# Optimization experiments

Hardware: AMD Instinct MI355X
Metric: run time of the kernel (lower is better)

## Reference

```python
import jax, jax.numpy as jnp
import numpy as np

N = 100000
E = 1600000
G = 256
D_IN = 128
NEURON = 64
ATT_F = 8
K = 3
ALPHA = 0.1


def setup_inputs() -> dict:
    key = jax.random.key(0)
    ks = jax.random.split(key, 12)
    x = jax.random.normal(ks[0], (N, D_IN), dtype=jnp.float32)
    closeness_feature = jax.random.normal(ks[1], (N, ATT_F), dtype=jnp.float32)
    edge_index = jax.random.randint(ks[2], (2, E), 0, N, dtype=jnp.int32)
    batch = jnp.sort(jax.random.randint(ks[3], (N,), 0, G, dtype=jnp.int32))
    s = 0.05
    return {
        "x": x,
        "closeness_feature": closeness_feature,
        "edge_index": edge_index,
        "batch": batch,
        "num_graphs": G,
        "nn1_w": jax.random.normal(ks[4], (D_IN, NEURON), dtype=jnp.float32) * s,
        "nn1_b": jnp.zeros((NEURON,), dtype=jnp.float32),
        "close_w": jax.random.normal(ks[5], (ATT_F, 1), dtype=jnp.float32) * s,
        "close_b": jnp.zeros((1,), dtype=jnp.float32),
        "att1_w": jax.random.normal(ks[6], (NEURON, 16), dtype=jnp.float32) * s,
        "att1_b": jnp.zeros((16,), dtype=jnp.float32),
        "att2_w": jax.random.normal(ks[7], (16, 1), dtype=jnp.float32) * s,
        "att2_b": jnp.zeros((1,), dtype=jnp.float32),
    }


def _appnp(x, edge_index, n):
    # gcn_norm with self-loops: A_hat = D^{-1/2}(A+I)D^{-1/2}
    loop = jnp.arange(n, dtype=edge_index.dtype)
    src = jnp.concatenate([edge_index[0], loop])
    dst = jnp.concatenate([edge_index[1], loop])
    deg = jax.ops.segment_sum(jnp.ones_like(dst, dtype=x.dtype), dst, num_segments=n)
    dinv = jax.lax.rsqrt(deg)  # deg >= 1 due to self loops
    norm = (dinv[src] * dinv[dst])[:, None]  # [E+N, 1]
    h = x
    for _ in range(K):
        agg = jax.ops.segment_sum(norm * h[src], dst, num_segments=n)
        h = (1.0 - ALPHA) * agg + ALPHA * x
    return h


def reference(x, closeness_feature, edge_index, batch, num_graphs,
              nn1_w, nn1_b, close_w, close_b, att1_w, att1_b, att2_w, att2_b):
    n = x.shape[0]
    h = _appnp(x, edge_index, n)                      # [N, D_IN]
    h = jax.nn.relu(h @ nn1_w + nn1_b)                # [N, 64]

    # per-graph softmax over closeness scores (segment softmax)
    logits = (closeness_feature @ close_w + close_b)[:, 0]          # [N]
    m = jax.ops.segment_max(logits, batch, num_segments=num_graphs)  # [G]
    w = jnp.exp(logits - m[batch])
    z = jax.ops.segment_sum(w, batch, num_segments=num_graphs)       # [G]
    p = w / z[batch]                                                 # softmax per graph

    cnt = jax.ops.segment_sum(jnp.ones((n,), dtype=h.dtype), batch,
                              num_segments=num_graphs)               # nodes per graph
    p = p * cnt[batch]                                               # scaled by curr_size

    # self_max: per-graph max over weighted node features
    pooled = jax.ops.segment_max(p[:, None] * h, batch, num_segments=num_graphs)  # [G, 64]

    a = jax.nn.relu(pooled @ att1_w + att1_b)         # [G, 16]
    return a @ att2_w + att2_b                        # [G, 1]
```

## Files before the change

### kernel.cpp

```cpp
#include <hip/hip_runtime.h>
#include <cstdint>
#include <cstddef>


#define DIN 128
#define NEU 64
#define BK2 512
#define BKSHIFT2 9
#define BKCAP 16384
#define ESCAP 12288
#define MAXNB 256

typedef __attribute__((ext_vector_type(8))) short short8v;
typedef __attribute__((ext_vector_type(4))) float f32x4;

__device__ inline float bf2f(unsigned short h) {
    return __uint_as_float(((unsigned)h) << 16);
}
__device__ inline unsigned short f2bf(float f) {
    unsigned u = __float_as_uint(f);
    unsigned r = u + 0x7FFFu + ((u >> 16) & 1u);
    return (unsigned short)(r >> 16);
}


__global__ __launch_bounds__(256) void binA_kernel(
        const int* __restrict__ src, const int* __restrict__ dst,
        int* __restrict__ bcur, int* __restrict__ pk, int E, int NB) {
    __shared__ int hist[MAXNB];
    __shared__ int cur[MAXNB];
    int nchunk = gridDim.x;
    int chunk = (E + nchunk - 1) / nchunk;
    int lo = blockIdx.x * chunk;
    int hi = min(E, lo + chunk);
    int t = threadIdx.x;
    for (int b = t; b < NB; b += 256) hist[b] = 0;
    __syncthreads();
    for (int i = lo + t; i < hi; i += 256)
        atomicAdd(&hist[dst[i] >> BKSHIFT2], 1);
    __syncthreads();
    for (int b = t; b < NB; b += 256)
        cur[b] = atomicAdd(&bcur[b], hist[b]);
    __syncthreads();
    for (int i = lo + t; i < hi; i += 256) {
        int d = dst[i];
        int b = d >> BKSHIFT2;
        int pos = atomicAdd(&cur[b], 1);
        pk[(size_t)b * BKCAP + pos] = (src[i] << BKSHIFT2) | (d & (BK2 - 1));
    }
}


__global__ void bscan_kernel(const int* __restrict__ bcur, int* __restrict__ bbase, int NB) {
    __shared__ int sh[256];
    int t = threadIdx.x;
    sh[t] = (t < NB) ? bcur[t] : 0;
    __syncthreads();
    for (int d = 1; d < 256; d <<= 1) {
        int v = (t >= d) ? sh[t - d] : 0;
        __syncthreads();
        sh[t] += v;
        __syncthreads();
    }
    if (t < NB) bbase[t + 1] = sh[t];
    if (t == 0) bbase[0] = 0;
}


__global__ __launch_bounds__(256) void binB_kernel(
        const int* __restrict__ bcur, const int* __restrict__ bbase,
        const int* __restrict__ pk, int* __restrict__ es,
        int* __restrict__ rowptr, float* __restrict__ dinv, int N, int NB) {
    __shared__ int cur[BK2];
    __shared__ int sh[256];
    __shared__ int esl[ESCAP];
    int b = blockIdx.x;
    int t = threadIdx.x;
    int node0 = b << BKSHIFT2;
    int count = bcur[b];
    int base = bbase[b];
    const int* pb = pk + (size_t)b * BKCAP;

    for (int v = t; v < BK2; v += 256) cur[v] = 0;
    __syncthreads();
    for (int i = t; i < count; i += 256)
        atomicAdd(&cur[pb[i] & (BK2 - 1)], 1);
    __syncthreads();
    int c0 = cur[2 * t], c1 = cur[2 * t + 1];
    int s = c0 + c1;
    sh[t] = s;
    __syncthreads();
    for (int d = 1; d < 256; d <<= 1) {
        int v = (t >= d) ? sh[t - d] : 0;
        __syncthreads();
        sh[t] += v;
        __syncthreads();
    }
    int excl = sh[t] - s;
    int n0 = node0 + 2 * t;
    if (n0 < N) {
        rowptr[n0 + 1] = base + excl + c0;
        dinv[n0] = rsqrtf((float)c0 + 1.0f);
    }
    if (n0 + 1 < N) {
        rowptr[n0 + 2] = base + excl + c0 + c1;
        dinv[n0 + 1] = rsqrtf((float)c1 + 1.0f);
    }
    if (b == 0 && t == 0) rowptr[0] = 0;
    __syncthreads();
    cur[2 * t] = excl;
    cur[2 * t + 1] = excl + c0;
    __syncthreads();
    for (int i = t; i < count; i += 256) {
        int v = pb[i];
        int pos = atomicAdd(&cur[v & (BK2 - 1)], 1);
        if (pos < ESCAP) esl[pos] = v >> BKSHIFT2;
    }
    __syncthreads();
    for (int i = t; i < count; i += 256) es[base + i] = esl[i];
}


__global__ __launch_bounds__(256) void fc1_kernel(
        const float* __restrict__ x, const float* __restrict__ W,
        ushort* __restrict__ yb, int N) {
    __shared__ ushort sW[DIN * NEU];
    int tid = threadIdx.x;
    for (int k = tid; k < DIN * NEU / 2; k += 256) {
        float2 v = ((const float2*)W)[k];
        ushort2 o;
        o.x = f2bf(v.x);
        o.y = f2bf(v.y);
        ((ushort2*)sW)[k] = o;
    }
    __syncthreads();
    int lane = tid & 63;
    int wv = tid >> 6;
    int l15 = lane & 15;
    int lg = lane >> 4;
    short8v bfrag[4][4];
#pragma unroll
    for (int kt = 0; kt < 4; kt++)
#pragma unroll
        for (int ct = 0; ct < 4; ct++) {
            short8v f;
#pragma unroll
            for (int e = 0; e < 8; e++)
                f[e] = (short)sW[(kt * 32 + lg * 8 + e) * NEU + ct * 16 + l15];
            bfrag[kt][ct] = f;
        }
    long long row0 = (long long)blockIdx.x * 64 + wv * 16;
    if (row0 >= N) return;
    bool rowok = (row0 + l15) < N;
    const float* xr = x + (size_t)(row0 + l15) * DIN;
    f32x4 acc[4];
#pragma unroll
    for (int ct = 0; ct < 4; ct++) acc[ct] = (f32x4){0.f, 0.f, 0.f, 0.f};
#pragma unroll
    for (int kt = 0; kt < 4; kt++) {
        short8v af = (short8v){0, 0, 0, 0, 0, 0, 0, 0};
        if (rowok) {
            float4 v0 = *((const float4*)(xr + kt * 32 + lg * 8));
            float4 v1 = *((const float4*)(xr + kt * 32 + lg * 8 + 4));
            af[0] = (short)f2bf(v0.x); af[1] = (short)f2bf(v0.y);
            af[2] = (short)f2bf(v0.z); af[3] = (short)f2bf(v0.w);
            af[4] = (short)f2bf(v1.x); af[5] = (short)f2bf(v1.y);
            af[6] = (short)f2bf(v1.z); af[7] = (short)f2bf(v1.w);
        }
#pragma unroll
        for (int ct = 0; ct < 4; ct++)
            acc[ct] = __builtin_amdgcn_mfma_f32_16x16x32_bf16(af, bfrag[kt][ct], acc[ct], 0, 0, 0);
    }
#pragma unroll
    for (int ct = 0; ct < 4; ct++)
#pragma unroll
        for (int r = 0; r < 4; r++) {
            long long rr = row0 + lg * 4 + r;
            if (rr < N) yb[(size_t)rr * NEU + ct * 16 + l15] = f2bf(acc[ct][r]);
        }
}


__global__ void scale_kernel(const ushort* __restrict__ yb, const float* __restrict__ dinv,
                             ushort* __restrict__ g0, ushort* __restrict__ g1,
                             ushort* __restrict__ g2, int N) {
    int i = blockIdx.x * blockDim.x + threadIdx.x;
    int stride = gridDim.x * blockDim.x;
    int total = N * 16;
    for (; i < total; i += stride) {
        int node = i >> 4;
        float dd = dinv[node];
        ushort4 v = ((const ushort4*)yb)[i];
        ushort4 o;
        o.x = f2bf(dd * bf2f(v.x));
        o.y = f2bf(dd * bf2f(v.y));
        o.z = f2bf(dd * bf2f(v.z));
        o.w = f2bf(dd * bf2f(v.w));
        ((ushort4*)g0)[i] = o;
    }
    if (blockIdx.x == 0 && threadIdx.x < 48) {
        int buf = threadIdx.x >> 4, e = threadIdx.x & 15;
        ushort* gp = (buf == 0) ? g0 : (buf == 1) ? g1 : g2;
        ((ushort4*)(gp + (size_t)N * NEU))[e] = make_ushort4(0, 0, 0, 0);
    }
}


template <int MODE>
__global__ __launch_bounds__(256) void pull_kernel(
        const int* __restrict__ rowptr, const int* __restrict__ es,
        const float* __restrict__ dinv, const ushort* __restrict__ gin,
        const ushort* __restrict__ yb, const float* __restrict__ b1,
        ushort* __restrict__ gout, float* __restrict__ h2out, int N) {
    int wid = threadIdx.x >> 6;
    int lane = threadIdx.x & 63;
    int quarter = lane >> 4;
    int l16 = lane & 15;
    int node = blockIdx.x * 4 + wid;
    if (node >= N) return;
    int beg = rowptr[node], end = rowptr[node + 1];
    float dd = dinv[node];
    float4 a0 = make_float4(0.f, 0.f, 0.f, 0.f);
    float4 a1 = make_float4(0.f, 0.f, 0.f, 0.f);
    float4 a2 = make_float4(0.f, 0.f, 0.f, 0.f);
    float4 a3 = make_float4(0.f, 0.f, 0.f, 0.f);
    int deg = end - beg;
    for (int base = 0; base < deg; base += 64) {
        int myi = base + lane;
        int msrc = (myi < deg) ? es[beg + myi] : N;
        int cnt = min(64, deg - base);
        int quads4 = (cnt + 15) >> 4;
        for (int j = 0; j < quads4; j++) {
            int i0 = 16 * j + quarter;
            int s0 = __shfl(msrc, i0);
            int s1 = __shfl(msrc, i0 + 4);
            int s2 = __shfl(msrc, i0 + 8);
            int s3 = __shfl(msrc, i0 + 12);
            ushort4 w0 = *((const ushort4*)(gin + (size_t)s0 * NEU) + l16);
            ushort4 w1 = *((const ushort4*)(gin + (size_t)s1 * NEU) + l16);
            ushort4 w2 = *((const ushort4*)(gin + (size_t)s2 * NEU) + l16);
            ushort4 w3 = *((const ushort4*)(gin + (size_t)s3 * NEU) + l16);
            a0.x += bf2f(w0.x); a0.y += bf2f(w0.y); a0.z += bf2f(w0.z); a0.w += bf2f(w0.w);
            a1.x += bf2f(w1.x); a1.y += bf2f(w1.y); a1.z += bf2f(w1.z); a1.w += bf2f(w1.w);
            a2.x += bf2f(w2.x); a2.y += bf2f(w2.y); a2.z += bf2f(w2.z); a2.w += bf2f(w2.w);
            a3.x += bf2f(w3.x); a3.y += bf2f(w3.y); a3.z += bf2f(w3.z); a3.w += bf2f(w3.w);
        }
    }
    float4 acc;
    acc.x = (a0.x + a1.x) + (a2.x + a3.x);
    acc.y = (a0.y + a1.y) + (a2.y + a3.y);
    acc.z = (a0.z + a1.z) + (a2.z + a3.z);
    acc.w = (a0.w + a1.w) + (a2.w + a3.w);
    acc.x += __shfl_xor(acc.x, 16);
    acc.y += __shfl_xor(acc.y, 16);
    acc.z += __shfl_xor(acc.z, 16);
    acc.w += __shfl_xor(acc.w, 16);
    acc.x += __shfl_xor(acc.x, 32);
    acc.y += __shfl_xor(acc.y, 32);
    acc.z += __shfl_xor(acc.z, 32);
    acc.w += __shfl_xor(acc.w, 32);
    if (quarter == 0) {
        ushort4 gv = *((const ushort4*)(gin + (size_t)node * NEU) + l16);
        ushort4 yv = *((const ushort4*)(yb + (size_t)node * NEU) + l16);
        float c9 = 0.9f * dd;
        float hx = c9 * (acc.x + bf2f(gv.x)) + 0.1f * bf2f(yv.x);
        float hy = c9 * (acc.y + bf2f(gv.y)) + 0.1f * bf2f(yv.y);
        float hz = c9 * (acc.z + bf2f(gv.z)) + 0.1f * bf2f(yv.z);
        float hw = c9 * (acc.w + bf2f(gv.w)) + 0.1f * bf2f(yv.w);
        if (MODE == 1) {
            float4 bb = *((const float4*)b1 + l16);
            float4 o;
            o.x = fmaxf(hx + bb.x, 0.f);
            o.y = fmaxf(hy + bb.y, 0.f);
            o.z = fmaxf(hz + bb.z, 0.f);
            o.w = fmaxf(hw + bb.w, 0.f);
            *((float4*)(h2out + (size_t)node * NEU) + l16) = o;
        } else {
            ushort4 o;
            o.x = f2bf(dd * hx); o.y = f2bf(dd * hy);
            o.z = f2bf(dd * hz); o.w = f2bf(dd * hw);
            *((ushort4*)(gout + (size_t)node * NEU) + l16) = o;
        }
    }
}


__global__ void logits_kernel(const float* __restrict__ cf, const float* __restrict__ cw,
                              const float* __restrict__ cb, float* __restrict__ logits, int N) {
    int i = blockIdx.x * blockDim.x + threadIdx.x;
    if (i >= N) return;
    const float4* c = (const float4*)(cf + (size_t)i * 8);
    float4 a = c[0], b = c[1];
    float s = a.x * cw[0] + a.y * cw[1] + a.z * cw[2] + a.w * cw[3]
            + b.x * cw[4] + b.y * cw[5] + b.z * cw[6] + b.w * cw[7] + cb[0];
    logits[i] = s;
}


__global__ void boundary_kernel(const int* __restrict__ batch, int* __restrict__ offs,
                                int N, int G) {
    int g = blockIdx.x * blockDim.x + threadIdx.x;
    if (g > G) return;
    int lo = 0, hi = N;
    while (lo < hi) {
        int mid = (lo + hi) >> 1;
        if (batch[mid] < g) lo = mid + 1; else hi = mid;
    }
    offs[g] = lo;
}


__global__ __launch_bounds__(256) void softmax_kernel(
        const float* __restrict__ logits, const int* __restrict__ offs,
        float* __restrict__ p, int G) {
    int g = blockIdx.x;
    int s0 = offs[g], e0 = offs[g + 1];
    int tid = threadIdx.x;
    __shared__ float red[256];
    float m = -INFINITY;
    for (int i = s0 + tid; i < e0; i += 256) m = fmaxf(m, logits[i]);
    red[tid] = m; __syncthreads();
    for (int w = 128; w > 0; w >>= 1) {
        if (tid < w) red[tid] = fmaxf(red[tid], red[tid + w]);
        __syncthreads();
    }
    m = red[0]; __syncthreads();
    float z = 0.f;
    for (int i = s0 + tid; i < e0; i += 256) z += expf(logits[i] - m);
    red[tid] = z; __syncthreads();
    for (int w = 128; w > 0; w >>= 1) {
        if (tid < w) red[tid] += red[tid + w];
        __syncthreads();
    }
    z = red[0];
    float scale = (float)(e0 - s0) / z;
    for (int i = s0 + tid; i < e0; i += 256) p[i] = expf(logits[i] - m) * scale;
}


__global__ __launch_bounds__(256) void pool_kernel(
        const float* __restrict__ h2, const float* __restrict__ p,
        const int* __restrict__ offs, float* __restrict__ pooled, int G) {
    int g = blockIdx.x;
    int s0 = offs[g], e0 = offs[g + 1];
    int tid = threadIdx.x;
    int j = tid & 63, r = tid >> 6;
    float mx = -INFINITY;
    for (int i = s0 + r; i < e0; i += 4)
        mx = fmaxf(mx, p[i] * h2[(size_t)i * NEU + j]);
    __shared__ float red[256];
    red[tid] = mx;
    __syncthreads();
    if (r == 0) {
        float m0 = fmaxf(fmaxf(red[j], red[64 + j]), fmaxf(red[128 + j], red[192 + j]));
        pooled[(size_t)g * NEU + j] = m0;
    }
}


__global__ void final_kernel(const float* __restrict__ pooled, const float* __restrict__ w1,
                             const float* __restrict__ b1, const float* __restrict__ w2,
                             const float* __restrict__ b2, float* __restrict__ out, int G) {
    int g = blockIdx.x;
    int tid = threadIdx.x;
    __shared__ float sp[64];
    __shared__ float sa[16];
    sp[tid] = pooled[(size_t)g * 64 + tid];
    __syncthreads();
    if (tid < 16) {
        float acc = b1[tid];
#pragma unroll
        for (int k = 0; k < 64; k++) acc = fmaf(sp[k], w1[k * 16 + tid], acc);
        sa[tid] = fmaxf(acc, 0.f);
    }
    __syncthreads();
    if (tid == 0) {
        float o = b2[0];
#pragma unroll
        for (int k = 0; k < 16; k++) o = fmaf(sa[k], w2[k], o);
        out[g] = o;
    }
}


extern "C" void kernel_launch(void* const* d_in, const int* in_sizes, int n_in,
                              void* d_out, int out_size, void* d_ws, size_t ws_size,
                              hipStream_t stream) {
    const float* x       = (const float*)d_in[0];
    const float* cf      = (const float*)d_in[1];
    const int*   ei      = (const int*)d_in[2];
    const int*   batch   = (const int*)d_in[3];
    const float* nn1_w   = (const float*)d_in[5];
    const float* nn1_b   = (const float*)d_in[6];
    const float* close_w = (const float*)d_in[7];
    const float* close_b = (const float*)d_in[8];
    const float* att1_w  = (const float*)d_in[9];
    const float* att1_b  = (const float*)d_in[10];
    const float* att2_w  = (const float*)d_in[11];
    const float* att2_b  = (const float*)d_in[12];
    float* out = (float*)d_out;

    int N = in_sizes[0] / DIN;
    int E = in_sizes[2] / 2;
    int G = out_size;

    const int* src = ei;
    const int* dst = ei + E;

    char* w = (char*)d_ws;
    size_t off = 0;
    auto alloc = [&](size_t bytes) -> void* {
        void* ptr = w + off;
        off += (bytes + 511) & ~(size_t)511;
        return ptr;
    };
    int NB = (N + BK2 - 1) >> BKSHIFT2;

    ushort* yb     = (ushort*)alloc((size_t)N * NEU * 2);
    ushort* g0     = (ushort*)alloc(((size_t)N + 1) * NEU * 2);
    ushort* g1     = (ushort*)alloc(((size_t)N + 1) * NEU * 2);
    ushort* g2     = (ushort*)alloc(((size_t)N + 1) * NEU * 2);
    float* h2      = (float*)alloc((size_t)N * NEU * 4);
    float* dinv    = (float*)alloc((size_t)N * 4);
    int*   rowptr  = (int*)alloc(((size_t)N + 1) * 4);
    int*   es      = (int*)alloc((size_t)E * 4);
    int*   bcur    = (int*)alloc((size_t)NB * 4);
    int*   bbase   = (int*)alloc(((size_t)NB + 1) * 4);
    int*   pk      = (int*)alloc((size_t)NB * BKCAP * 4);
    float* logits  = (float*)alloc((size_t)N * 4);
    float* p       = (float*)alloc((size_t)N * 4);
    int*   offs    = (int*)alloc(((size_t)G + 1) * 4);
    float* pooled  = (float*)alloc((size_t)G * NEU * 4);
    (void)ws_size; (void)n_in;

    hipMemsetAsync(bcur, 0, (size_t)NB * 4, stream);

    binA_kernel<<<256, 256, 0, stream>>>(src, dst, bcur, pk, E, NB);
    bscan_kernel<<<1, 256, 0, stream>>>(bcur, bbase, NB);
    binB_kernel<<<NB, 256, 0, stream>>>(bcur, bbase, pk, es, rowptr, dinv, N, NB);

    fc1_kernel<<<(N + 63) / 64, 256, 0, stream>>>(x, nn1_w, yb, N);
    scale_kernel<<<2048, 256, 0, stream>>>(yb, dinv, g0, g1, g2, N);

    pull_kernel<0><<<(N + 3) / 4, 256, 0, stream>>>(rowptr, es, dinv, g0, yb, nn1_b, g1, nullptr, N);
    pull_kernel<0><<<(N + 3) / 4, 256, 0, stream>>>(rowptr, es, dinv, g1, yb, nn1_b, g2, nullptr, N);
    pull_kernel<1><<<(N + 3) / 4, 256, 0, stream>>>(rowptr, es, dinv, g2, yb, nn1_b, nullptr, h2, N);

    logits_kernel<<<(N + 255) / 256, 256, 0, stream>>>(cf, close_w, close_b, logits, N);
    boundary_kernel<<<2, 256, 0, stream>>>(batch, offs, N, G);
    softmax_kernel<<<G, 256, 0, stream>>>(logits, offs, p, G);
    pool_kernel<<<G, 256, 0, stream>>>(h2, p, offs, pooled, G);
    final_kernel<<<G, 64, 0, stream>>>(pooled, att1_w, att1_b, att2_w, att2_b, out, G);
}
```

Before: 239.5 us.

## Fuse scale into fc1, merge head kernels, simplify pull gather unroll

Writes the dinv-scaled g0 directly from the fc1 epilogue, which removes the separate scale kernel and its reread of yb. Five head kernels (logits, boundary, softmax, pool, final) become one per-graph kernel that uses an online max/sum softmax and recomputes logits inline, cutting launches and intermediate buffers. The pull gather loop is narrowed from four to two independent loads per iteration and uses 32-bit indexing. This lowers memory-level parallelism in the gather, and the fast __expf adds some numerical risk.

```diff
diff --git a/kernel.cpp b/kernel.cpp
--- a/kernel.cpp
+++ b/kernel.cpp
@@ -123,9 +123,16 @@
 
 __global__ __launch_bounds__(256) void fc1_kernel(
         const float* __restrict__ x, const float* __restrict__ W,
-        ushort* __restrict__ yb, int N) {
+        const float* __restrict__ dinv, ushort* __restrict__ yb,
+        ushort* __restrict__ g0, ushort* __restrict__ g1,
+        ushort* __restrict__ g2, int N) {
+    int tid = threadIdx.x;
+    if (blockIdx.x == 0 && tid < 48) {
+        int buf = tid >> 4, e = tid & 15;
+        ushort* gp = (buf == 0) ? g0 : (buf == 1) ? g1 : g2;
+        ((ushort4*)(gp + (size_t)N * NEU))[e] = make_ushort4(0, 0, 0, 0);
+    }
     __shared__ ushort sW[DIN * NEU];
-    int tid = threadIdx.x;
     for (int k = tid; k < DIN * NEU / 2; k += 256) {
         float2 v = ((const float2*)W)[k];
         ushort2 o;
@@ -172,36 +179,17 @@
             acc[ct] = __builtin_amdgcn_mfma_f32_16x16x32_bf16(af, bfrag[kt][ct], acc[ct], 0, 0, 0);
     }
 #pragma unroll
-    for (int ct = 0; ct < 4; ct++)
-#pragma unroll
-        for (int r = 0; r < 4; r++) {
-            long long rr = row0 + lg * 4 + r;
-            if (rr < N) yb[(size_t)rr * NEU + ct * 16 + l15] = f2bf(acc[ct][r]);
-        }
-}
-
-
-__global__ void scale_kernel(const ushort* __restrict__ yb, const float* __restrict__ dinv,
-                             ushort* __restrict__ g0, ushort* __restrict__ g1,
-                             ushort* __restrict__ g2, int N) {
-    int i = blockIdx.x * blockDim.x + threadIdx.x;
-    int stride = gridDim.x * blockDim.x;
-    int total = N * 16;
-    for (; i < total; i += stride) {
-        int node = i >> 4;
-        float dd = dinv[node];
-        ushort4 v = ((const ushort4*)yb)[i];
-        ushort4 o;
-        o.x = f2bf(dd * bf2f(v.x));
-        o.y = f2bf(dd * bf2f(v.y));
-        o.z = f2bf(dd * bf2f(v.z));
-        o.w = f2bf(dd * bf2f(v.w));
-        ((ushort4*)g0)[i] = o;
-    }
-    if (blockIdx.x == 0 && threadIdx.x < 48) {
-        int buf = threadIdx.x >> 4, e = threadIdx.x & 15;
-        ushort* gp = (buf == 0) ? g0 : (buf == 1) ? g1 : g2;
-        ((ushort4*)(gp + (size_t)N * NEU))[e] = make_ushort4(0, 0, 0, 0);
+    for (int r = 0; r < 4; r++) {
+        long long rr = row0 + lg * 4 + r;
+        if (rr < N) {
+            float dv = dinv[rr];
+#pragma unroll
+            for (int ct = 0; ct < 4; ct++) {
+                float v = acc[ct][r];
+                yb[(size_t)rr * NEU + ct * 16 + l15] = f2bf(v);
+                g0[(size_t)rr * NEU + ct * 16 + l15] = f2bf(dv * v);
+            }
+        }
     }
 }
 
@@ -220,37 +208,35 @@
     if (node >= N) return;
     int beg = rowptr[node], end = rowptr[node + 1];
     float dd = dinv[node];
+    const ushort4* gin4 = (const ushort4*)gin;
     float4 a0 = make_float4(0.f, 0.f, 0.f, 0.f);
     float4 a1 = make_float4(0.f, 0.f, 0.f, 0.f);
-    float4 a2 = make_float4(0.f, 0.f, 0.f, 0.f);
-    float4 a3 = make_float4(0.f, 0.f, 0.f, 0.f);
     int deg = end - beg;
     for (int base = 0; base < deg; base += 64) {
         int myi = base + lane;
         int msrc = (myi < deg) ? es[beg + myi] : N;
         int cnt = min(64, deg - base);
-        int quads4 = (cnt + 15) >> 4;
-        for (int j = 0; j < quads4; j++) {
-            int i0 = 16 * j + quarter;
-            int s0 = __shfl(msrc, i0);
-            int s1 = __shfl(msrc, i0 + 4);
-            int s2 = __shfl(msrc, i0 + 8);
-            int s3 = __shfl(msrc, i0 + 12);
-            ushort4 w0 = *((const ushort4*)(gin + (size_t)s0 * NEU) + l16);
-            ushort4 w1 = *((const ushort4*)(gin + (size_t)s1 * NEU) + l16);
-            ushort4 w2 = *((const ushort4*)(gin + (size_t)s2 * NEU) + l16);
-            ushort4 w3 = *((const ushort4*)(gin + (size_t)s3 * NEU) + l16);
+        int quads = (cnt + 3) >> 2;
+        int j = 0;
+        for (; j + 1 < quads; j += 2) {
+            int s0 = __shfl(msrc, 4 * j + quarter);
+            int s1 = __shfl(msrc, 4 * j + 4 + quarter);
+            ushort4 w0 = gin4[(uint)(s0 << 4) + l16];
+            ushort4 w1 = gin4[(uint)(s1 << 4) + l16];
             a0.x += bf2f(w0.x); a0.y += bf2f(w0.y); a0.z += bf2f(w0.z); a0.w += bf2f(w0.w);
             a1.x += bf2f(w1.x); a1.y += bf2f(w1.y); a1.z += bf2f(w1.z); a1.w += bf2f(w1.w);
-            a2.x += bf2f(w2.x); a2.y += bf2f(w2.y); a2.z += bf2f(w2.z); a2.w += bf2f(w2.w);
-            a3.x += bf2f(w3.x); a3.y += bf2f(w3.y); a3.z += bf2f(w3.z); a3.w += bf2f(w3.w);
+        }
+        if (j < quads) {
+            int s0 = __shfl(msrc, 4 * j + quarter);
+            ushort4 w0 = gin4[(uint)(s0 << 4) + l16];
+            a0.x += bf2f(w0.x); a0.y += bf2f(w0.y); a0.z += bf2f(w0.z); a0.w += bf2f(w0.w);
         }
     }
     float4 acc;
-    acc.x = (a0.x + a1.x) + (a2.x + a3.x);
-    acc.y = (a0.y + a1.y) + (a2.y + a3.y);
-    acc.z = (a0.z + a1.z) + (a2.z + a3.z);
-    acc.w = (a0.w + a1.w) + (a2.w + a3.w);
+    acc.x = a0.x + a1.x;
+    acc.y = a0.y + a1.y;
+    acc.z = a0.z + a1.z;
+    acc.w = a0.w + a1.w;
     acc.x += __shfl_xor(acc.x, 16);
     acc.y += __shfl_xor(acc.y, 16);
     acc.z += __shfl_xor(acc.z, 16);
@@ -285,99 +271,86 @@
 }
 
 
-__global__ void logits_kernel(const float* __restrict__ cf, const float* __restrict__ cw,
-                              const float* __restrict__ cb, float* __restrict__ logits, int N) {
-    int i = blockIdx.x * blockDim.x + threadIdx.x;
-    if (i >= N) return;
-    const float4* c = (const float4*)(cf + (size_t)i * 8);
-    float4 a = c[0], b = c[1];
-    float s = a.x * cw[0] + a.y * cw[1] + a.z * cw[2] + a.w * cw[3]
-            + b.x * cw[4] + b.y * cw[5] + b.z * cw[6] + b.w * cw[7] + cb[0];
-    logits[i] = s;
-}
-
-
-__global__ void boundary_kernel(const int* __restrict__ batch, int* __restrict__ offs,
-                                int N, int G) {
-    int g = blockIdx.x * blockDim.x + threadIdx.x;
-    if (g > G) return;
-    int lo = 0, hi = N;
-    while (lo < hi) {
-        int mid = (lo + hi) >> 1;
-        if (batch[mid] < g) lo = mid + 1; else hi = mid;
-    }
-    offs[g] = lo;
-}
-
-
-__global__ __launch_bounds__(256) void softmax_kernel(
-        const float* __restrict__ logits, const int* __restrict__ offs,
-        float* __restrict__ p, int G) {
+__global__ __launch_bounds__(256) void head_kernel(
+        const int* __restrict__ batch, const float* __restrict__ cf,
+        const float* __restrict__ cw, const float* __restrict__ cb,
+        const float* __restrict__ h2, const float* __restrict__ aw1,
+        const float* __restrict__ ab1, const float* __restrict__ aw2,
+        const float* __restrict__ ab2, float* __restrict__ out, int N) {
     int g = blockIdx.x;
-    int s0 = offs[g], e0 = offs[g + 1];
     int tid = threadIdx.x;
-    __shared__ float red[256];
-    float m = -INFINITY;
-    for (int i = s0 + tid; i < e0; i += 256) m = fmaxf(m, logits[i]);
-    red[tid] = m; __syncthreads();
+    __shared__ int sbound[2];
+    __shared__ float redm[256];
+    __shared__ float redz[256];
+    __shared__ float pooled[64];
+    __shared__ float sa[16];
+    if (tid < 2) {
+        int target = g + tid;
+        int lo = 0, hi = N;
+        while (lo < hi) {
+            int mid = (lo + hi) >> 1;
+            if (batch[mid] < target) lo = mid + 1; else hi = mid;
+        }
+        sbound[tid] = lo;
+    }
+    __syncthreads();
+    int s0 = sbound[0], e0 = sbound[1];
+    float w0 = cw[0], w1 = cw[1], w2 = cw[2], w3 = cw[3];
+    float w4 = cw[4], w5 = cw[5], w6 = cw[6], w7 = cw[7];
+    float cb0 = cb[0];
+    float m = -INFINITY, z = 0.f;
+    for (int i = s0 + tid; i < e0; i += 256) {
+        const float4* c = (const float4*)(cf + (size_t)i * 8);
+        float4 A = c[0], B = c[1];
+        float l = A.x * w0 + A.y * w1 + A.z * w2 + A.w * w3
+                + B.x * w4 + B.y * w5 + B.z * w6 + B.w * w7 + cb0;
+        float mn = fmaxf(m, l);
+        z = z * __expf(m - mn) + __expf(l - mn);
+        m = mn;
+    }
+    redm[tid] = m; redz[tid] = z;
+    __syncthreads();
     for (int w = 128; w > 0; w >>= 1) {
-        if (tid < w) red[tid] = fmaxf(red[tid], red[tid + w]);
+        if (tid < w) {
+            float ma = redm[tid], mb = redm[tid + w];
+            float za = redz[tid], zb = redz[tid + w];
+            float mn = fmaxf(ma, mb);
+            redz[tid] = (mn == -INFINITY) ? 0.f
+                       : za * __expf(ma - mn) + zb * __expf(mb - mn);
+            redm[tid] = mn;
+        }
         __syncthreads();
     }
-    m = red[0]; __syncthreads();
-    float z = 0.f;
-    for (int i = s0 + tid; i < e0; i += 256) z += expf(logits[i] - m);
-    red[tid] = z; __syncthreads();
-    for (int w = 128; w > 0; w >>= 1) {
-        if (tid < w) red[tid] += red[tid + w];
-        __syncthreads();
-    }
-    z = red[0];
-    float scale = (float)(e0 - s0) / z;
-    for (int i = s0 + tid; i < e0; i += 256) p[i] = expf(logits[i] - m) * scale;
-}
-
-
-__global__ __launch_bounds__(256) void pool_kernel(
-        const float* __restrict__ h2, const float* __restrict__ p,
-        const int* __restrict__ offs, float* __restrict__ pooled, int G) {
-    int g = blockIdx.x;
-    int s0 = offs[g], e0 = offs[g + 1];
-    int tid = threadIdx.x;
+    float M = redm[0];
+    float scale = (float)(e0 - s0) / redz[0];
+    __syncthreads();
     int j = tid & 63, r = tid >> 6;
     float mx = -INFINITY;
-    for (int i = s0 + r; i < e0; i += 4)
-        mx = fmaxf(mx, p[i] * h2[(size_t)i * NEU + j]);
-    __shared__ float red[256];
-    red[tid] = mx;
-    __syncthreads();
-    if (r == 0) {
-        float m0 = fmaxf(fmaxf(red[j], red[64 + j]), fmaxf(red[128 + j], red[192 + j]));
-        pooled[(size_t)g * NEU + j] = m0;
-    }
-}
-
-
-__global__ void final_kernel(const float* __restrict__ pooled, const float* __restrict__ w1,
-                             const float* __restrict__ b1, const float* __restrict__ w2,
-                             const float* __restrict__ b2, float* __restrict__ out, int G) {
-    int g = blockIdx.x;
-    int tid = threadIdx.x;
-    __shared__ float sp[64];
-    __shared__ float sa[16];
-    sp[tid] = pooled[(size_t)g * 64 + tid];
+    for (int i = s0 + r; i < e0; i += 4) {
+        const float4* c = (const float4*)(cf + (size_t)i * 8);
+        float4 A = c[0], B = c[1];
+        float l = A.x * w0 + A.y * w1 + A.z * w2 + A.w * w3
+                + B.x * w4 + B.y * w5 + B.z * w6 + B.w * w7 + cb0;
+        float p = __expf(l - M) * scale;
+        mx = fmaxf(mx, p * h2[(size_t)i * NEU + j]);
+    }
+    redm[tid] = mx;
+    __syncthreads();
+    if (r == 0)
+        pooled[j] = fmaxf(fmaxf(redm[j], redm[64 + j]),
+                          fmaxf(redm[128 + j], redm[192 + j]));
     __syncthreads();
     if (tid < 16) {
-        float acc = b1[tid];
-#pragma unroll
-        for (int k = 0; k < 64; k++) acc = fmaf(sp[k], w1[k * 16 + tid], acc);
+        float acc = ab1[tid];
+#pragma unroll
+        for (int k = 0; k < 64; k++) acc = fmaf(pooled[k], aw1[k * 16 + tid], acc);
         sa[tid] = fmaxf(acc, 0.f);
     }
     __syncthreads();
     if (tid == 0) {
-        float o = b2[0];
-#pragma unroll
-        for (int k = 0; k < 16; k++) o = fmaf(sa[k], w2[k], o);
+        float o = ab2[0];
+#pragma unroll
+        for (int k = 0; k < 16; k++) o = fmaf(sa[k], aw2[k], o);
         out[g] = o;
     }
 }
@@ -427,10 +400,6 @@
     int*   bcur    = (int*)alloc((size_t)NB * 4);
     int*   bbase   = (int*)alloc(((size_t)NB + 1) * 4);
     int*   pk      = (int*)alloc((size_t)NB * BKCAP * 4);
-    float* logits  = (float*)alloc((size_t)N * 4);
-    float* p       = (float*)alloc((size_t)N * 4);
-    int*   offs    = (int*)alloc(((size_t)G + 1) * 4);
-    float* pooled  = (float*)alloc((size_t)G * NEU * 4);
     (void)ws_size; (void)n_in;
 
     hipMemsetAsync(bcur, 0, (size_t)NB * 4, stream);
@@ -439,16 +408,12 @@
     bscan_kernel<<<1, 256, 0, stream>>>(bcur, bbase, NB);
     binB_kernel<<<NB, 256, 0, stream>>>(bcur, bbase, pk, es, rowptr, dinv, N, NB);
 
-    fc1_kernel<<<(N + 63) / 64, 256, 0, stream>>>(x, nn1_w, yb, N);
-    scale_kernel<<<2048, 256, 0, stream>>>(yb, dinv, g0, g1, g2, N);
+    fc1_kernel<<<(N + 63) / 64, 256, 0, stream>>>(x, nn1_w, dinv, yb, g0, g1, g2, N);
 
     pull_kernel<0><<<(N + 3) / 4, 256, 0, stream>>>(rowptr, es, dinv, g0, yb, nn1_b, g1, nullptr, N);
     pull_kernel<0><<<(N + 3) / 4, 256, 0, stream>>>(rowptr, es, dinv, g1, yb, nn1_b, g2, nullptr, N);
     pull_kernel<1><<<(N + 3) / 4, 256, 0, stream>>>(rowptr, es, dinv, g2, yb, nn1_b, nullptr, h2, N);
 
-    logits_kernel<<<(N + 255) / 256, 256, 0, stream>>>(cf, close_w, close_b, logits, N);
-    boundary_kernel<<<2, 256, 0, stream>>>(batch, offs, N, G);
-    softmax_kernel<<<G, 256, 0, stream>>>(logits, offs, p, G);
-    pool_kernel<<<G, 256, 0, stream>>>(h2, p, offs, pooled, G);
-    final_kernel<<<G, 64, 0, stream>>>(pooled, att1_w, att1_b, att2_w, att2_b, out, G);
-}
+    head_kernel<<<G, 256, 0, stream>>>(batch, cf, close_w, close_b, h2,
+                                       att1_w, att1_b, att2_w, att2_b, out, N);
+}
```

Result: no change. 242.7 us (+1.4%).
